# Kernel tuning notes

Hardware: AMD Instinct MI355X
Metric: run time of the kernel (lower is better)

The kernel has to match this reference:

```python
import jax, jax.numpy as jnp
import numpy as np

N_HEADS = 8
N_POINTS = 4
LN_EPS = 1e-5


def _ln(x, g, b):
    m = jnp.mean(x, -1, keepdims=True)
    v = jnp.mean((x - m) ** 2, -1, keepdims=True)
    return (x - m) * jax.lax.rsqrt(v + LN_EPS) * g + b


def _mha(q, k, v, wq, bq, wk, bk, wv, bv, wo, bo):
    B, Lq, C = q.shape
    Dh = C // N_HEADS
    Q = (q @ wq.T + bq).reshape(B, Lq, N_HEADS, Dh)
    K = (k @ wk.T + bk).reshape(B, -1, N_HEADS, Dh)
    V = (v @ wv.T + bv).reshape(B, -1, N_HEADS, Dh)
    s = jnp.einsum('bqhd,bkhd->bhqk', Q, K) * (1.0 / float(np.sqrt(Dh)))
    a = jax.nn.softmax(s, -1)
    o = jnp.einsum('bhqk,bkhd->bqhd', a, V).reshape(B, Lq, C)
    return o @ wo.T + bo


def _ref_points(h, w, L):
    ry = jnp.linspace(0.5, h - 0.5, h) / h
    rx = jnp.linspace(0.5, w - 0.5, w) / w
    gy, gx = jnp.meshgrid(ry, rx, indexing='ij')
    ref = jnp.stack([gx.reshape(-1), gy.reshape(-1)], -1)[None]  # (1, h*w, 2)
    return jnp.broadcast_to(ref[:, :, None, :], (1, h * w, L, 2))


def _deform_core(value, shapes, starts, loc, aw):
    # value: (B, Len_in, H, Dh); loc: (B, Lq, H, L, P, 2); aw: (B, Lq, H, L, P)
    B, _, H, Dh = value.shape
    Lq, P = loc.shape[1], loc.shape[4]
    out = jnp.zeros((B, H, Lq, Dh), value.dtype)
    for l in range(shapes.shape[0]):
        Hl, Wl = int(shapes[l, 0]), int(shapes[l, 1])
        s = int(starts[l])
        v = value[:, s:s + Hl * Wl].transpose(0, 2, 1, 3)  # (B, H, Hl*Wl, Dh)
        # grid_sample(align_corners=False, padding_mode='zeros') pixel coords
        xl = loc[:, :, :, l, :, 0] * Wl - 0.5  # (B, Lq, H, P)
        yl = loc[:, :, :, l, :, 1] * Hl - 0.5
        x0 = jnp.floor(xl); y0 = jnp.floor(yl)
        fx = xl - x0; fy = yl - y0
        x0 = x0.astype(jnp.int32); y0 = y0.astype(jnp.int32)
        acc = jnp.zeros((B, H, Lq, P, Dh), value.dtype)
        for dy, dx in ((0, 0), (0, 1), (1, 0), (1, 1)):
            xi = x0 + dx; yi = y0 + dy
            wgt = (fx if dx else 1.0 - fx) * (fy if dy else 1.0 - fy)
            valid = ((xi >= 0) & (xi < Wl) & (yi >= 0) & (yi < Hl)).astype(value.dtype)
            idx = (jnp.clip(yi, 0, Hl - 1) * Wl + jnp.clip(xi, 0, Wl - 1))
            idx = idx.transpose(0, 2, 1, 3).reshape(B, H, Lq * P)
            g = jnp.take_along_axis(v, idx[..., None], axis=2).reshape(B, H, Lq, P, Dh)
            acc = acc + g * (wgt * valid).transpose(0, 2, 1, 3)[..., None]
        out = out + jnp.einsum('bhqpd,bqhp->bhqd', acc, aw[:, :, :, l])
    return out.transpose(0, 2, 1, 3).reshape(B, Lq, H * Dh)


def reference(tgt, query_pos, src, wq, bq, wk, bk, wv, bv, wo, bo, ln2_g, ln2_b,
              w_off, b_off, w_attn, b_attn, w_val, b_val, w_cout, b_cout,
              ln1_g, ln1_b, w1, b1, w2, b2, ln3_g, ln3_b,
              src_spatial_shapes, level_start_index, h, w):
    shapes = np.asarray(src_spatial_shapes)
    starts = np.asarray(level_start_index)
    h = int(h); w = int(w)
    L = shapes.shape[0]
    B, Lq, C = tgt.shape
    Dh = C // N_HEADS
    # --- self attention (post-LN residual) ---
    q = tgt + query_pos
    t2 = _mha(q, q, tgt, wq, bq, wk, bk, wv, bv, wo, bo)
    t = _ln(tgt + t2, ln2_g, ln2_b)
    # --- MSDeformAttn cross attention ---
    qc = t + query_pos
    value = (src @ w_val.T + b_val).reshape(B, -1, N_HEADS, Dh)
    off = (qc @ w_off.T + b_off).reshape(B, Lq, N_HEADS, L, N_POINTS, 2)
    aw = (qc @ w_attn.T + b_attn).reshape(B, Lq, N_HEADS, L * N_POINTS)
    aw = jax.nn.softmax(aw, -1).reshape(B, Lq, N_HEADS, L, N_POINTS)
    norm = jnp.stack([shapes[:, 1].astype(np.float32), shapes[:, 0].astype(np.float32)], -1)  # (L,2): (W,H)
    rp = _ref_points(h, w, L)  # (1, Lq, L, 2)
    loc = rp[:, :, None, :, None, :] + off / norm[None, None, None, :, None, :]
    samp = _deform_core(value, shapes, starts, loc, aw)
    t2 = samp @ w_cout.T + b_cout
    t = _ln(t + t2, ln1_g, ln1_b)
    # --- FFN ---
    t2 = jax.nn.relu(t @ w1.T + b1) @ w2.T + b2
    t = _ln(t + t2, ln3_g, ln3_b)
    return t


def setup_inputs() -> dict:
    key = jax.random.key(0)
    B, C, L, P, dff = 2, 256, 4, 4, 1024
    h = w = 48
    shapes = np.array([[48, 48], [24, 24], [12, 12], [6, 6]], np.int32)
    starts = np.array([0, 2304, 2880, 3024], np.int32)
    Len_in = 3060
    Lq = h * w
    ks = iter(jax.random.split(key, 40))
    def rn(shape, s=0.02):
        return jax.random.normal(next(ks), shape, jnp.float32) * s
    return dict(
        tgt=rn((B, Lq, C), 1.0), query_pos=rn((B, Lq, C), 1.0), src=rn((B, Len_in, C), 1.0),
        wq=rn((C, C)), bq=rn((C,)), wk=rn((C, C)), bk=rn((C,)), wv=rn((C, C)), bv=rn((C,)),
        wo=rn((C, C)), bo=rn((C,)),
        ln2_g=jnp.ones((C,)), ln2_b=jnp.zeros((C,)),
        w_off=rn((N_HEADS * L * P * 2, C)), b_off=rn((N_HEADS * L * P * 2,)),
        w_attn=rn((N_HEADS * L * P, C)), b_attn=rn((N_HEADS * L * P,)),
        w_val=rn((C, C)), b_val=rn((C,)), w_cout=rn((C, C)), b_cout=rn((C,)),
        ln1_g=jnp.ones((C,)), ln1_b=jnp.zeros((C,)),
        w1=rn((dff, C)), b1=rn((dff,)), w2=rn((C, dff)), b2=rn((C,)),
        ln3_g=jnp.ones((C,)), ln3_b=jnp.zeros((C,)),
        src_spatial_shapes=shapes, level_start_index=starts, h=h, w=w)
```

## Files before the change

### kernel.cpp

```cpp
#include <hip/hip_runtime.h>
#include <hip/hip_bf16.h>
#include <math.h>

typedef __hip_bfloat16 bf16;
typedef __attribute__((ext_vector_type(8))) short short8;
typedef __attribute__((ext_vector_type(4))) short short4v;
typedef __attribute__((ext_vector_type(4))) float f32x4;

static constexpr int B   = 2;
static constexpr int LQ  = 2304;
static constexpr int C   = 256;
static constexpr int NH  = 8;
static constexpr int DH  = 32;
static constexpr int NL  = 4;
static constexpr int NP  = 4;
static constexpr int LEN = 3060;
static constexpr int DFF = 1024;
static constexpr int MQ  = B * LQ;
static constexpr int MV  = B * LEN;
static constexpr int SZ1 = MQ * C;

#define MFMA16(a, b, c) __builtin_amdgcn_mfma_f32_16x16x32_bf16(a, b, c, 0, 0, 0)

__device__ __forceinline__ float ldf(const void* p, size_t i, int bf) {
  return bf ? __bfloat162float(((const bf16*)p)[i]) : ((const float*)p)[i];
}
__device__ __forceinline__ short fl2s(float v) {
  bf16 h = __float2bfloat16(v);
  return *(short*)&h;
}
__device__ __forceinline__ short fl2s_fast(float v) {
  union { float f; unsigned u; } x; x.f = v;
  return (short)((x.u + 0x8000u) >> 16);
}
__device__ __forceinline__ float s2fl(short s) {
  return __bfloat162float(*(bf16*)&s);
}
__device__ __forceinline__ int wire_is_bf16(const unsigned* gprobe) {
  return gprobe[0] == 0x3F803F80u;
}

static constexpr int CVN = 20;
__device__ const int g_cvt_cnt[CVN] = {
  65536, 65536, 256, 256, 65536, 256, 65536, 256,
  65536, 32768, 256, 128, 65536, 256, 65536, 256,
  262144, 1024, 262144, 256};
__device__ const int g_cvt_off[CVN] = {
  0, 65536, 131072, 131328, 131584, 197120, 197376, 262912,
  263168, 328704, 361472, 361728, 361856, 427392, 427648, 493184,
  493440, 755584, 756608, 1018752};
static constexpr int CV_WQ = 0, CV_WK = 65536, CV_BQ = 131072, CV_BK = 131328;
static constexpr int CV_WV = 131584, CV_BV = 197120;
static constexpr int CV_WO = 197376, CV_BO = 262912;
static constexpr int CV_WOFF = 263168, CV_WATTN = 328704;
static constexpr int CV_BOFF = 361472, CV_BATTN = 361728;
static constexpr int CV_WVAL = 361856, CV_BVAL = 427392;
static constexpr int CV_WCOUT = 427648, CV_BCOUT = 493184;
static constexpr int CV_W1 = 493440, CV_B1 = 755584;
static constexpr int CV_W2 = 756608, CV_B2 = 1018752;
static constexpr int CV_TOTAL = 1019008;

struct CvtArgs { const void* p[22]; };

__global__ __launch_bounds__(256) void prep_all(CvtArgs a, const void* __restrict__ qpos,
                                                short* __restrict__ cvt,
                                                short* __restrict__ tgt16,
                                                short* __restrict__ q16,
                                                short* __restrict__ src16,
                                                const unsigned* __restrict__ gprobe) {
  const int fl = wire_is_bf16(gprobe);
  const int seg = blockIdx.y;
  if (fl && seg != 20) return;
  const int cnt = (seg < 20) ? g_cvt_cnt[seg] : (seg == 20 ? SZ1 : MV * C);
  const int stride = gridDim.x * 256;
  for (int i = blockIdx.x * 256 + threadIdx.x; i < cnt; i += stride) {
    if (seg < 20) {
      cvt[g_cvt_off[seg] + i] = fl2s(((const float*)a.p[seg])[i]);
    } else if (seg == 20) {
      float t = ldf(a.p[20], i, fl);
      if (!fl) tgt16[i] = fl2s(t);
      q16[i] = fl2s(t + ldf(qpos, i, fl));
    } else {
      src16[i] = fl2s(((const float*)a.p[21])[i]);
    }
  }
}

struct GemmJob {
  int Xmode;
  const short* Xbf; const void* Xwire;
  const short* Wcvt; const short* bcvt;
  const void* Wwire; const void* bwire;
  void* Y;
  int M, N, K, ldY, col0, relu, out_mode, nblk_x;
  float qscale;
};
struct GemmBatch { GemmJob j[4]; int start[5]; int njobs; };

__global__ __launch_bounds__(256) void gemm_mfma(GemmBatch nb,
                                                 const unsigned* __restrict__ gprobe) {
  const int fl = wire_is_bf16(gprobe);
  int id = blockIdx.x;
  int jj = 0;
  while (jj + 1 < nb.njobs && id >= nb.start[jj + 1]) ++jj;
  const GemmJob jb = nb.j[jj];
  const short* Xsel = (jb.Xmode && fl) ? (const short*)jb.Xwire : jb.Xbf;
  const short* Wsel = fl ? (const short*)jb.Wwire : jb.Wcvt;
  const short* bsel = fl ? (const short*)jb.bwire : jb.bcvt;
  const int local = id - nb.start[jj];
  const int bx = local % jb.nblk_x;
  const int by = local / jb.nblk_x;
  const int M = jb.M, N = jb.N, K = jb.K;

  __shared__ short Xs[128][72];
  __shared__ short Ws[64][72];
  const int tid = threadIdx.x;
  const int wave = tid >> 6, lane = tid & 63;
  const int quad = lane >> 4, l16 = lane & 15;
  const int m0 = bx * 128, n0 = by * 64;
  f32x4 acc[2][4];
#pragma unroll
  for (int mt = 0; mt < 2; ++mt)
#pragma unroll
    for (int nt = 0; nt < 4; ++nt) acc[mt][nt] = f32x4{0.f, 0.f, 0.f, 0.f};

  const int xrow = tid >> 1;
  const int xcol = (tid & 1) * 32;
  const int wrow = tid >> 2;
  const int wcol = (tid & 3) * 16;
  int xr = m0 + xrow; if (xr >= M) xr = M - 1;
  const short* xp = Xsel + (size_t)xr * K;
  const short* wp = Wsel + (size_t)(n0 + wrow) * K;

  for (int k0 = 0; k0 < K; k0 += 64) {
#pragma unroll
    for (int u = 0; u < 4; ++u)
      *(short8*)&Xs[xrow][xcol + u * 8] = *(const short8*)(xp + k0 + xcol + u * 8);
    *(short8*)&Ws[wrow][wcol]     = *(const short8*)(wp + k0 + wcol);
    *(short8*)&Ws[wrow][wcol + 8] = *(const short8*)(wp + k0 + wcol + 8);
    __syncthreads();
#pragma unroll
    for (int kc = 0; kc < 2; ++kc) {
#pragma unroll
      for (int mt = 0; mt < 2; ++mt) {
        short8 a = *(const short8*)&Xs[wave * 32 + mt * 16 + l16][kc * 32 + quad * 8];
#pragma unroll
        for (int nt = 0; nt < 4; ++nt) {
          short8 b = *(const short8*)&Ws[nt * 16 + l16][kc * 32 + quad * 8];
          acc[mt][nt] = MFMA16(a, b, acc[mt][nt]);
        }
      }
    }
    __syncthreads();
  }

  if (jb.out_mode == 2) {
#pragma unroll
    for (int mt = 0; mt < 2; ++mt) {
      const int mbase = m0 + wave * 32 + mt * 16 + quad * 4;
      const int b = mbase / LQ;
      const int qb_ = mbase - b * LQ;
#pragma unroll
      for (int nt = 0; nt < 4; ++nt) {
        const int n = n0 + nt * 16 + l16;
        const float bv = s2fl(bsel[n]);
        short4v v4;
#pragma unroll
        for (int r = 0; r < 4; ++r) v4[r] = fl2s(acc[mt][nt][r] + bv);
        *(short4v*)((short*)jb.Y + (size_t)(b * 256 + n) * LQ + qb_) = v4;
      }
    }
    return;
  }
#pragma unroll
  for (int mt = 0; mt < 2; ++mt)
#pragma unroll
    for (int nt = 0; nt < 4; ++nt) {
      const int n = n0 + nt * 16 + l16;
      const float bv = s2fl(bsel[n]);
#pragma unroll
      for (int r = 0; r < 4; ++r) {
        const int m = m0 + wave * 32 + mt * 16 + quad * 4 + r;
        if (m < M) {
          float v = (acc[mt][nt][r] + bv) * jb.qscale;
          if (jb.relu) v = fmaxf(v, 0.f);
          if (jb.out_mode == 1)
            ((short*)jb.Y)[(size_t)m * jb.ldY + jb.col0 + n] = fl2s(v);
          else
            ((float*)jb.Y)[(size_t)m * jb.ldY + jb.col0 + n] = v;
        }
      }
    }
}

__global__ __launch_bounds__(256) void flash_attn(const short* __restrict__ QK,
                                                  const short* __restrict__ Vt,
                                                  short* __restrict__ Op) {
  constexpr int LDQK = 512;
  constexpr int NC = LQ / 64;
  constexpr int NQT = 3;
  const int qb = blockIdx.x;
  const int bh = blockIdx.y;
  const int b = bh >> 3, h = bh & 7;
  const int tid = threadIdx.x;
  const int wave = tid >> 6, lane = tid & 63;
  const int quad = lane >> 4, l16 = lane & 15;

  __shared__ short Ps[4][16][68];
  __shared__ float lsh[256];

  const int q0 = qb * 48;
  const size_t rowb = (size_t)(b * LQ);
  const short* kcol = QK + 256 + h * DH + quad * 8;
  const short* vt0 = Vt + (size_t)(b * 256 + h * 32 + l16) * LQ + quad * 8;
  const short* vt1 = Vt + (size_t)(b * 256 + h * 32 + 16 + l16) * LQ + quad * 8;

  short8 qfrag[NQT];
#pragma unroll
  for (int qt = 0; qt < NQT; ++qt)
    qfrag[qt] = *(const short8*)(QK + (rowb + q0 + qt * 16 + l16) * LDQK + h * DH + quad * 8);

  f32x4 o0[NQT], o1[NQT];
  float lrow[NQT];
#pragma unroll
  for (int qt = 0; qt < NQT; ++qt) {
    o0[qt] = f32x4{0.f, 0.f, 0.f, 0.f};
    o1[qt] = f32x4{0.f, 0.f, 0.f, 0.f};
    lrow[qt] = 0.f;
  }

  short8 kf[4], vf[4];
  {
    const int k0 = wave * 64;
#pragma unroll
    for (int kt = 0; kt < 4; ++kt)
      kf[kt] = *(const short8*)(kcol + (rowb + k0 + kt * 16 + l16) * LDQK);
    vf[0] = *(const short8*)(vt0 + k0);
    vf[1] = *(const short8*)(vt0 + k0 + 32);
    vf[2] = *(const short8*)(vt1 + k0);
    vf[3] = *(const short8*)(vt1 + k0 + 32);
  }

  for (int c = wave; c < NC; c += 4) {
    short8 kn[4], vn[4];
    if (c + 4 < NC) {
      const int k0n = (c + 4) * 64;
#pragma unroll
      for (int kt = 0; kt < 4; ++kt)
        kn[kt] = *(const short8*)(kcol + (rowb + k0n + kt * 16 + l16) * LDQK);
      vn[0] = *(const short8*)(vt0 + k0n);
      vn[1] = *(const short8*)(vt0 + k0n + 32);
      vn[2] = *(const short8*)(vt1 + k0n);
      vn[3] = *(const short8*)(vt1 + k0n + 32);
    }

#pragma unroll
    for (int qt = 0; qt < NQT; ++qt) {
      f32x4 s[4];
#pragma unroll
      for (int kt = 0; kt < 4; ++kt) {
        f32x4 z = {0.f, 0.f, 0.f, 0.f};
        s[kt] = MFMA16(kf[kt], qfrag[qt], z);
      }

      float ps = 0.f;
#pragma unroll
      for (int kt = 0; kt < 4; ++kt)
#pragma unroll
        for (int r = 0; r < 4; ++r) {
          float p = __expf(s[kt][r]);
          s[kt][r] = p;
          ps += p;
        }
      lrow[qt] += ps;

#pragma unroll
      for (int kt = 0; kt < 4; ++kt) {
        short4v pk;
#pragma unroll
        for (int r = 0; r < 4; ++r) pk[r] = fl2s_fast(s[kt][r]);
        *(short4v*)&Ps[wave][l16][kt * 16 + quad * 4] = pk;
      }

#pragma unroll
      for (int half = 0; half < 2; ++half) {
        short4v a0 = *(const short4v*)&Ps[wave][l16][half * 32 + quad * 8];
        short4v a1 = *(const short4v*)&Ps[wave][l16][half * 32 + quad * 8 + 4];
        short8 afrag;
#pragma unroll
        for (int j = 0; j < 4; ++j) { afrag[j] = a0[j]; afrag[4 + j] = a1[j]; }
        o0[qt] = MFMA16(afrag, vf[half], o0[qt]);
        o1[qt] = MFMA16(afrag, vf[2 + half], o1[qt]);
      }
    }

#pragma unroll
    for (int kt = 0; kt < 4; ++kt) { kf[kt] = kn[kt]; vf[kt] = vn[kt]; }
  }

  float* obuf = (float*)&Ps[0][0][0];
  for (int qt = 0; qt < NQT; ++qt) {
    __syncthreads();
    lsh[(wave * 4 + quad) * 16 + l16] = lrow[qt];
#pragma unroll
    for (int r = 0; r < 4; ++r) {
      const int q = quad * 4 + r;
      obuf[(wave * 16 + q) * 32 + l16] = o0[qt][r];
      obuf[(wave * 16 + q) * 32 + 16 + l16] = o1[qt][r];
    }
    __syncthreads();
#pragma unroll
    for (int e = tid; e < 512; e += 256) {
      const int q = e >> 5, d = e & 31;
      float lg = 0.f;
#pragma unroll
      for (int i = 0; i < 16; ++i) lg += lsh[i * 16 + q];
      float ov = 0.f;
#pragma unroll
      for (int w = 0; w < 4; ++w) ov += obuf[(w * 16 + q) * 32 + d];
      Op[(rowb + q0 + qt * 16 + q) * C + h * DH + d] = fl2s_fast(ov / lg);
    }
  }
}

__global__ __launch_bounds__(256) void ln_kern(const void* __restrict__ A, int a_mode,
                                               const float* __restrict__ R,
                                               const void* __restrict__ g,
                                               const void* __restrict__ be,
                                               float* __restrict__ Yf32,
                                               short* __restrict__ Y16,
                                               void* __restrict__ Yfinal,
                                               const void* __restrict__ pos,
                                               short* __restrict__ Yqc,
                                               int rows, const unsigned* __restrict__ gprobe) {
  const int fl = wire_is_bf16(gprobe);
  const int row = blockIdx.x * 4 + (threadIdx.x >> 6);
  const int lane = threadIdx.x & 63;
  if (row >= rows) return;
  float x[4], s = 0.f, s2 = 0.f;
#pragma unroll
  for (int u = 0; u < 4; ++u) {
    int c = lane + 64 * u;
    size_t idx = (size_t)row * C + c;
    float a = (a_mode == 1) ? ldf(A, idx, fl) : ((const float*)A)[idx];
    x[u] = a + R[idx];
    s += x[u];
    s2 += x[u] * x[u];
  }
#pragma unroll
  for (int off = 32; off > 0; off >>= 1) {
    s += __shfl_xor(s, off);
    s2 += __shfl_xor(s2, off);
  }
  const float mean = s * (1.f / C);
  const float var = fmaxf(s2 * (1.f / C) - mean * mean, 0.f);
  const float inv = rsqrtf(var + 1e-5f);
#pragma unroll
  for (int u = 0; u < 4; ++u) {
    int c = lane + 64 * u;
    size_t idx = (size_t)row * C + c;
    float y = (x[u] - mean) * inv * ldf(g, c, fl) + ldf(be, c, fl);
    if (Yfinal) {
      if (fl) ((short*)Yfinal)[idx] = fl2s(y);
      else ((float*)Yfinal)[idx] = y;
    } else {
      if (Yf32) Yf32[idx] = y;
      if (Y16) Y16[idx] = fl2s(y);
      if (Yqc) Yqc[idx] = fl2s(y + ldf(pos, idx, fl));
    }
  }
}

__global__ __launch_bounds__(256) void deform_kern(const short* __restrict__ value,
                                                   const float* __restrict__ oa,
                                                   const int* __restrict__ shapes,
                                                   const int* __restrict__ starts,
                                                   const int* __restrict__ hp,
                                                   const int* __restrict__ wp,
                                                   short* __restrict__ samp) {
  const int bq = blockIdx.x * 4 + (threadIdx.x >> 6);
  const int b = bq / LQ, q = bq % LQ;
  const int lane = threadIdx.x & 63;
  const int h_ = lane >> 3;
  const int d0 = (lane & 7) * 4;

  const int w0 = *wp, h0 = *hp;
  const int qx = q % w0, qy = q / w0;
  const float refx = (qx + 0.5f) / (float)w0;
  const float refy = (qy + 0.5f) / (float)h0;

  const float* offp = oa + (size_t)bq * 384 + h_ * 32;
  const float* awraw = oa + (size_t)bq * 384 + 256 + h_ * 16;

  float e[16];
  float mm = -1e30f;
#pragma unroll
  for (int j = 0; j < 16; ++j) mm = fmaxf(mm, awraw[j]);
  float ssum = 0.f;
#pragma unroll
  for (int j = 0; j < 16; ++j) {
    e[j] = __expf(awraw[j] - mm);
    ssum += e[j];
  }
  const float sinv = 1.f / ssum;

  float acc0 = 0.f, acc1 = 0.f, acc2 = 0.f, acc3 = 0.f;
  for (int l = 0; l < NL; ++l) {
    const int Hl = shapes[l * 2 + 0];
    const int Wl = shapes[l * 2 + 1];
    const int st = starts[l];
    const short* vbase = value + ((size_t)(b * LEN + st)) * C + h_ * DH + d0;
#pragma unroll
    for (int p = 0; p < NP; ++p) {
      const float ox = offp[l * 8 + p * 2 + 0];
      const float oy = offp[l * 8 + p * 2 + 1];
      const float a = e[l * 4 + p] * sinv;
      const float xl = refx * Wl + ox - 0.5f;
      const float yl = refy * Hl + oy - 0.5f;
      const float x0f = floorf(xl), y0f = floorf(yl);
      const float fx = xl - x0f, fy = yl - y0f;
      const int x0 = (int)x0f, y0 = (int)y0f;
#pragma unroll
      for (int corner = 0; corner < 4; ++corner) {
        const int dx = corner & 1, dy = corner >> 1;
        const int xi = x0 + dx, yi = y0 + dy;
        const float wx = dx ? fx : 1.f - fx;
        const float wy = dy ? fy : 1.f - fy;
        const bool valid = (xi >= 0) & (xi < Wl) & (yi >= 0) & (yi < Hl);
        if (valid) {
          const float w = a * wx * wy;
          short4v v4 = *(const short4v*)(vbase + (size_t)(yi * Wl + xi) * C);
          acc0 += w * s2fl(v4[0]);
          acc1 += w * s2fl(v4[1]);
          acc2 += w * s2fl(v4[2]);
          acc3 += w * s2fl(v4[3]);
        }
      }
    }
  }
  short4v out;
  out[0] = fl2s(acc0); out[1] = fl2s(acc1); out[2] = fl2s(acc2); out[3] = fl2s(acc3);
  *(short4v*)(samp + (size_t)bq * C + h_ * DH + d0) = out;
}

extern "C" void kernel_launch(void* const* d_in, const int* in_sizes, int n_in,
                              void* d_out, int out_size, void* d_ws, size_t ws_size,
                              hipStream_t stream) {
  const void* tgt       = d_in[0];
  const void* query_pos = d_in[1];
  const void* src       = d_in[2];
  const void* wq = d_in[3];  const void* bq = d_in[4];
  const void* wk = d_in[5];  const void* bk = d_in[6];
  const void* wv = d_in[7];  const void* bv = d_in[8];
  const void* wo = d_in[9];  const void* bo = d_in[10];
  const void* ln2_g = d_in[11]; const void* ln2_b = d_in[12];
  const void* w_off = d_in[13]; const void* b_off = d_in[14];
  const void* w_attn = d_in[15]; const void* b_attn = d_in[16];
  const void* w_val = d_in[17]; const void* b_val = d_in[18];
  const void* w_cout = d_in[19]; const void* b_cout = d_in[20];
  const void* ln1_g = d_in[21]; const void* ln1_b = d_in[22];
  const void* w1 = d_in[23]; const void* b1 = d_in[24];
  const void* w2 = d_in[25]; const void* b2 = d_in[26];
  const void* ln3_g = d_in[27]; const void* ln3_b = d_in[28];
  const int* shapes = (const int*)d_in[29];
  const int* starts = (const int*)d_in[30];
  const int* hp = (const int*)d_in[31];
  const int* wp = (const int*)d_in[32];
  const unsigned* gprobe = (const unsigned*)ln2_g;

  short* cvt    = (short*)((char*)d_ws + 256);
  short* tgt16  = cvt + CV_TOTAL;
  short* q16    = tgt16 + SZ1;
  short* src16  = q16 + SZ1;
  short* qk_out = src16 + (size_t)MV * C;
  short* vt16   = qk_out + (size_t)MQ * 512;
  short* ao16   = vt16 + SZ1;
  short* valb   = ao16 + SZ1;
  short* ffn1   = valb + (size_t)MV * C;
  short* t1_16  = ffn1 + (size_t)MQ * DFF;
  float* t2a    = (float*)(t1_16 + SZ1);
  float* t_32   = t2a + SZ1;
  float* t1_32  = t_32 + SZ1;
  float* oa     = t1_32 + SZ1;

  const float scale = 1.f / sqrtf((float)DH);
  const dim3 blk(256);
  const int NXQ = MQ / 128;
  const int NXV = (MV + 127) / 128;

  CvtArgs ca;
  ca.p[0] = wq;  ca.p[1] = wk;  ca.p[2] = bq;  ca.p[3] = bk;
  ca.p[4] = wv;  ca.p[5] = bv;  ca.p[6] = wo;  ca.p[7] = bo;
  ca.p[8] = w_off; ca.p[9] = w_attn; ca.p[10] = b_off; ca.p[11] = b_attn;
  ca.p[12] = w_val; ca.p[13] = b_val; ca.p[14] = w_cout; ca.p[15] = b_cout;
  ca.p[16] = w1; ca.p[17] = b1; ca.p[18] = w2; ca.p[19] = b2;
  ca.p[20] = tgt; ca.p[21] = src;
  prep_all<<<dim3(192, 22), blk, 0, stream>>>(ca, query_pos, cvt, tgt16, q16, src16, gprobe);

  {
    GemmBatch nb;
    nb.njobs = 4;
    nb.j[0] = {0, q16, nullptr, cvt + CV_WQ, cvt + CV_BQ, wq, bq, qk_out,
               MQ, 256, 256, 512, 0, 0, 1, NXQ, scale};
    nb.j[1] = {0, q16, nullptr, cvt + CV_WK, cvt + CV_BK, wk, bk, qk_out,
               MQ, 256, 256, 512, 256, 0, 1, NXQ, 1.f};
    nb.j[2] = {2, tgt16, tgt, cvt + CV_WV, cvt + CV_BV, wv, bv, vt16,
               MQ, 256, 256, 0, 0, 0, 2, NXQ, 1.f};
    nb.j[3] = {3, src16, src, cvt + CV_WVAL, cvt + CV_BVAL, w_val, b_val, valb,
               MV, 256, 256, 256, 0, 0, 1, NXV, 1.f};
    nb.start[0] = 0;
    nb.start[1] = NXQ * 4;
    nb.start[2] = nb.start[1] + NXQ * 4;
    nb.start[3] = nb.start[2] + NXQ * 4;
    nb.start[4] = nb.start[3] + NXV * 4;
    gemm_mfma<<<nb.start[4], blk, 0, stream>>>(nb, gprobe);
  }
  flash_attn<<<dim3(LQ / 48, B * NH), blk, 0, stream>>>(qk_out, vt16, ao16);
  {
    GemmBatch nb;
    nb.njobs = 1;
    nb.j[0] = {0, ao16, nullptr, cvt + CV_WO, cvt + CV_BO, wo, bo, t2a,
               MQ, 256, 256, 256, 0, 0, 0, NXQ, 1.f};
    nb.start[0] = 0; nb.start[1] = NXQ * 4;
    gemm_mfma<<<nb.start[1], blk, 0, stream>>>(nb, gprobe);
  }
  ln_kern<<<MQ / 4, blk, 0, stream>>>(tgt, 1, t2a, ln2_g, ln2_b,
                                      t_32, nullptr, nullptr, query_pos, q16, MQ, gprobe);

  {
    GemmBatch nb;
    nb.njobs = 2;
    nb.j[0] = {0, q16, nullptr, cvt + CV_WOFF, cvt + CV_BOFF, w_off, b_off, oa,
               MQ, 256, 256, 384, 0, 0, 0, NXQ, 1.f};
    nb.j[1] = {0, q16, nullptr, cvt + CV_WATTN, cvt + CV_BATTN, w_attn, b_attn, oa,
               MQ, 128, 256, 384, 256, 0, 0, NXQ, 1.f};
    nb.start[0] = 0;
    nb.start[1] = NXQ * 4;
    nb.start[2] = nb.start[1] + NXQ * 2;
    gemm_mfma<<<nb.start[2], blk, 0, stream>>>(nb, gprobe);
  }
  deform_kern<<<MQ / 4, blk, 0, stream>>>(valb, oa, shapes, starts, hp, wp, ao16);
  {
    GemmBatch nb;
    nb.njobs = 1;
    nb.j[0] = {0, ao16, nullptr, cvt + CV_WCOUT, cvt + CV_BCOUT, w_cout, b_cout, t2a,
               MQ, 256, 256, 256, 0, 0, 0, NXQ, 1.f};
    nb.start[0] = 0; nb.start[1] = NXQ * 4;
    gemm_mfma<<<nb.start[1], blk, 0, stream>>>(nb, gprobe);
  }
  ln_kern<<<MQ / 4, blk, 0, stream>>>(t_32, 2, t2a, ln1_g, ln1_b,
                                      t1_32, t1_16, nullptr, nullptr, nullptr, MQ, gprobe);

  {
    GemmBatch nb;
    nb.njobs = 1;
    nb.j[0] = {0, t1_16, nullptr, cvt + CV_W1, cvt + CV_B1, w1, b1, ffn1,
               MQ, 1024, 256, 1024, 0, 1, 1, NXQ, 1.f};
    nb.start[0] = 0; nb.start[1] = NXQ * 16;
    gemm_mfma<<<nb.start[1], blk, 0, stream>>>(nb, gprobe);
  }
  {
    GemmBatch nb;
    nb.njobs = 1;
    nb.j[0] = {0, ffn1, nullptr, cvt + CV_W2, cvt + CV_B2, w2, b2, t2a,
               MQ, 256, 1024, 256, 0, 0, 0, NXQ, 1.f};
    nb.start[0] = 0; nb.start[1] = NXQ * 4;
    gemm_mfma<<<nb.start[1], blk, 0, stream>>>(nb, gprobe);
  }
  ln_kern<<<MQ / 4, blk, 0, stream>>>(t1_32, 2, t2a, ln3_g, ln3_b,
                                      nullptr, nullptr, d_out, nullptr, nullptr, MQ, gprobe);
}
```

Measured before the change: 284.2 us.

## Fuse tgt+query_pos add into QK GEMM loads and use 64-row tiles for N=256 GEMMs

In bf16-wire mode the prep kernel now exits early. The Q/K projection GEMM reads tgt and query_pos directly and adds them while staging the X tile into shared memory, which removes a separate elementwise pass. The GEMM is templated on its M tile size, and the smaller GEMMs (output projection, offset/attention, cout, FFN2) now use 64-row tiles to launch twice as many blocks for better CU occupancy. The prep grid is also halved. In exchange, each Q/K block redoes the bf16 add per N tile, and smaller tiles reuse each weight tile less.

```diff
diff --git a/kernel.cpp b/kernel.cpp
--- a/kernel.cpp
+++ b/kernel.cpp
@@ -38,6 +38,12 @@
 }
 __device__ __forceinline__ int wire_is_bf16(const unsigned* gprobe) {
   return gprobe[0] == 0x3F803F80u;
+}
+__device__ __forceinline__ short8 add2bf(short8 a, short8 b) {
+  short8 r;
+#pragma unroll
+  for (int j = 0; j < 8; ++j) r[j] = fl2s(s2fl(a[j]) + s2fl(b[j]));
+  return r;
 }
 
 static constexpr int CVN = 20;
@@ -68,18 +74,17 @@
                                                 short* __restrict__ q16,
                                                 short* __restrict__ src16,
                                                 const unsigned* __restrict__ gprobe) {
-  const int fl = wire_is_bf16(gprobe);
+  if (wire_is_bf16(gprobe)) return;
   const int seg = blockIdx.y;
-  if (fl && seg != 20) return;
   const int cnt = (seg < 20) ? g_cvt_cnt[seg] : (seg == 20 ? SZ1 : MV * C);
   const int stride = gridDim.x * 256;
   for (int i = blockIdx.x * 256 + threadIdx.x; i < cnt; i += stride) {
     if (seg < 20) {
       cvt[g_cvt_off[seg] + i] = fl2s(((const float*)a.p[seg])[i]);
     } else if (seg == 20) {
-      float t = ldf(a.p[20], i, fl);
-      if (!fl) tgt16[i] = fl2s(t);
-      q16[i] = fl2s(t + ldf(qpos, i, fl));
+      float t = ((const float*)a.p[20])[i];
+      tgt16[i] = fl2s(t);
+      q16[i] = fl2s(t + ((const float*)qpos)[i]);
     } else {
       src16[i] = fl2s(((const float*)a.p[21])[i]);
     }
@@ -88,7 +93,7 @@
 
 struct GemmJob {
   int Xmode;
-  const short* Xbf; const void* Xwire;
+  const short* Xbf; const void* Xwire; const void* Xwire2;
   const short* Wcvt; const short* bcvt;
   const void* Wwire; const void* bwire;
   void* Y;
@@ -97,14 +102,18 @@
 };
 struct GemmBatch { GemmJob j[4]; int start[5]; int njobs; };
 
+template <int MR>
 __global__ __launch_bounds__(256) void gemm_mfma(GemmBatch nb,
                                                  const unsigned* __restrict__ gprobe) {
+  constexpr int MT = MR / 64;
   const int fl = wire_is_bf16(gprobe);
   int id = blockIdx.x;
   int jj = 0;
   while (jj + 1 < nb.njobs && id >= nb.start[jj + 1]) ++jj;
   const GemmJob jb = nb.j[jj];
-  const short* Xsel = (jb.Xmode && fl) ? (const short*)jb.Xwire : jb.Xbf;
+  const bool qcf = (jb.Xmode == 4) && fl;
+  const short* Xsel = jb.Xbf;
+  if ((jb.Xmode == 2 || jb.Xmode == 3) && fl) Xsel = (const short*)jb.Xwire;
   const short* Wsel = fl ? (const short*)jb.Wwire : jb.Wcvt;
   const short* bsel = fl ? (const short*)jb.bwire : jb.bcvt;
   const int local = id - nb.start[jj];
@@ -112,38 +121,50 @@
   const int by = local / jb.nblk_x;
   const int M = jb.M, N = jb.N, K = jb.K;
 
-  __shared__ short Xs[128][72];
+  __shared__ short Xs[MR][72];
   __shared__ short Ws[64][72];
   const int tid = threadIdx.x;
   const int wave = tid >> 6, lane = tid & 63;
   const int quad = lane >> 4, l16 = lane & 15;
-  const int m0 = bx * 128, n0 = by * 64;
-  f32x4 acc[2][4];
-#pragma unroll
-  for (int mt = 0; mt < 2; ++mt)
+  const int m0 = bx * MR, n0 = by * 64;
+  f32x4 acc[MT][4];
+#pragma unroll
+  for (int mt = 0; mt < MT; ++mt)
 #pragma unroll
     for (int nt = 0; nt < 4; ++nt) acc[mt][nt] = f32x4{0.f, 0.f, 0.f, 0.f};
 
-  const int xrow = tid >> 1;
-  const int xcol = (tid & 1) * 32;
+  const int xrow = (MR == 128) ? (tid >> 1) : (tid >> 2);
+  const int xcol = (MR == 128) ? ((tid & 1) * 32) : ((tid & 3) * 16);
+  constexpr int XU = (MR == 128) ? 4 : 2;
   const int wrow = tid >> 2;
   const int wcol = (tid & 3) * 16;
   int xr = m0 + xrow; if (xr >= M) xr = M - 1;
-  const short* xp = Xsel + (size_t)xr * K;
+  const short* xp = qcf ? nullptr : (Xsel + (size_t)xr * K);
+  const short* tp = qcf ? ((const short*)jb.Xwire + (size_t)xr * K) : nullptr;
+  const short* pp = qcf ? ((const short*)jb.Xwire2 + (size_t)xr * K) : nullptr;
   const short* wp = Wsel + (size_t)(n0 + wrow) * K;
 
   for (int k0 = 0; k0 < K; k0 += 64) {
-#pragma unroll
-    for (int u = 0; u < 4; ++u)
-      *(short8*)&Xs[xrow][xcol + u * 8] = *(const short8*)(xp + k0 + xcol + u * 8);
+    if (qcf) {
+#pragma unroll
+      for (int u = 0; u < XU; ++u) {
+        short8 t8 = *(const short8*)(tp + k0 + xcol + u * 8);
+        short8 p8 = *(const short8*)(pp + k0 + xcol + u * 8);
+        *(short8*)&Xs[xrow][xcol + u * 8] = add2bf(t8, p8);
+      }
+    } else {
+#pragma unroll
+      for (int u = 0; u < XU; ++u)
+        *(short8*)&Xs[xrow][xcol + u * 8] = *(const short8*)(xp + k0 + xcol + u * 8);
+    }
     *(short8*)&Ws[wrow][wcol]     = *(const short8*)(wp + k0 + wcol);
     *(short8*)&Ws[wrow][wcol + 8] = *(const short8*)(wp + k0 + wcol + 8);
     __syncthreads();
 #pragma unroll
     for (int kc = 0; kc < 2; ++kc) {
 #pragma unroll
-      for (int mt = 0; mt < 2; ++mt) {
-        short8 a = *(const short8*)&Xs[wave * 32 + mt * 16 + l16][kc * 32 + quad * 8];
+      for (int mt = 0; mt < MT; ++mt) {
+        short8 a = *(const short8*)&Xs[wave * (16 * MT) + mt * 16 + l16][kc * 32 + quad * 8];
 #pragma unroll
         for (int nt = 0; nt < 4; ++nt) {
           short8 b = *(const short8*)&Ws[nt * 16 + l16][kc * 32 + quad * 8];
@@ -156,8 +177,8 @@
 
   if (jb.out_mode == 2) {
 #pragma unroll
-    for (int mt = 0; mt < 2; ++mt) {
-      const int mbase = m0 + wave * 32 + mt * 16 + quad * 4;
+    for (int mt = 0; mt < MT; ++mt) {
+      const int mbase = m0 + wave * (16 * MT) + mt * 16 + quad * 4;
       const int b = mbase / LQ;
       const int qb_ = mbase - b * LQ;
 #pragma unroll
@@ -173,14 +194,14 @@
     return;
   }
 #pragma unroll
-  for (int mt = 0; mt < 2; ++mt)
+  for (int mt = 0; mt < MT; ++mt)
 #pragma unroll
     for (int nt = 0; nt < 4; ++nt) {
       const int n = n0 + nt * 16 + l16;
       const float bv = s2fl(bsel[n]);
 #pragma unroll
       for (int r = 0; r < 4; ++r) {
-        const int m = m0 + wave * 32 + mt * 16 + quad * 4 + r;
+        const int m = m0 + wave * (16 * MT) + mt * 16 + quad * 4 + r;
         if (m < M) {
           float v = (acc[mt][nt][r] + bv) * jb.qscale;
           if (jb.relu) v = fmaxf(v, 0.f);
@@ -485,8 +506,9 @@
 
   const float scale = 1.f / sqrtf((float)DH);
   const dim3 blk(256);
-  const int NXQ = MQ / 128;
-  const int NXV = (MV + 127) / 128;
+  const int NX128 = MQ / 128;
+  const int NX64  = MQ / 64;
+  const int NXV   = (MV + 127) / 128;
 
   CvtArgs ca;
   ca.p[0] = wq;  ca.p[1] = wk;  ca.p[2] = bq;  ca.p[3] = bk;
@@ -495,34 +517,34 @@
   ca.p[12] = w_val; ca.p[13] = b_val; ca.p[14] = w_cout; ca.p[15] = b_cout;
   ca.p[16] = w1; ca.p[17] = b1; ca.p[18] = w2; ca.p[19] = b2;
   ca.p[20] = tgt; ca.p[21] = src;
-  prep_all<<<dim3(192, 22), blk, 0, stream>>>(ca, query_pos, cvt, tgt16, q16, src16, gprobe);
+  prep_all<<<dim3(96, 22), blk, 0, stream>>>(ca, query_pos, cvt, tgt16, q16, src16, gprobe);
 
   {
     GemmBatch nb;
     nb.njobs = 4;
-    nb.j[0] = {0, q16, nullptr, cvt + CV_WQ, cvt + CV_BQ, wq, bq, qk_out,
-               MQ, 256, 256, 512, 0, 0, 1, NXQ, scale};
-    nb.j[1] = {0, q16, nullptr, cvt + CV_WK, cvt + CV_BK, wk, bk, qk_out,
-               MQ, 256, 256, 512, 256, 0, 1, NXQ, 1.f};
-    nb.j[2] = {2, tgt16, tgt, cvt + CV_WV, cvt + CV_BV, wv, bv, vt16,
-               MQ, 256, 256, 0, 0, 0, 2, NXQ, 1.f};
-    nb.j[3] = {3, src16, src, cvt + CV_WVAL, cvt + CV_BVAL, w_val, b_val, valb,
+    nb.j[0] = {4, q16, tgt, query_pos, cvt + CV_WQ, cvt + CV_BQ, wq, bq, qk_out,
+               MQ, 256, 256, 512, 0, 0, 1, NX128, scale};
+    nb.j[1] = {4, q16, tgt, query_pos, cvt + CV_WK, cvt + CV_BK, wk, bk, qk_out,
+               MQ, 256, 256, 512, 256, 0, 1, NX128, 1.f};
+    nb.j[2] = {2, tgt16, tgt, nullptr, cvt + CV_WV, cvt + CV_BV, wv, bv, vt16,
+               MQ, 256, 256, 0, 0, 0, 2, NX128, 1.f};
+    nb.j[3] = {3, src16, src, nullptr, cvt + CV_WVAL, cvt + CV_BVAL, w_val, b_val, valb,
                MV, 256, 256, 256, 0, 0, 1, NXV, 1.f};
     nb.start[0] = 0;
-    nb.start[1] = NXQ * 4;
-    nb.start[2] = nb.start[1] + NXQ * 4;
-    nb.start[3] = nb.start[2] + NXQ * 4;
+    nb.start[1] = NX128 * 4;
+    nb.start[2] = nb.start[1] + NX128 * 4;
+    nb.start[3] = nb.start[2] + NX128 * 4;
     nb.start[4] = nb.start[3] + NXV * 4;
-    gemm_mfma<<<nb.start[4], blk, 0, stream>>>(nb, gprobe);
+    gemm_mfma<128><<<nb.start[4], blk, 0, stream>>>(nb, gprobe);
   }
   flash_attn<<<dim3(LQ / 48, B * NH), blk, 0, stream>>>(qk_out, vt16, ao16);
   {
     GemmBatch nb;
     nb.njobs = 1;
-    nb.j[0] = {0, ao16, nullptr, cvt + CV_WO, cvt + CV_BO, wo, bo, t2a,
-               MQ, 256, 256, 256, 0, 0, 0, NXQ, 1.f};
-    nb.start[0] = 0; nb.start[1] = NXQ * 4;
-    gemm_mfma<<<nb.start[1], blk, 0, stream>>>(nb, gprobe);
+    nb.j[0] = {0, ao16, nullptr, nullptr, cvt + CV_WO, cvt + CV_BO, wo, bo, t2a,
+               MQ, 256, 256, 256, 0, 0, 0, NX64, 1.f};
+    nb.start[0] = 0; nb.start[1] = NX64 * 4;
+    gemm_mfma<64><<<nb.start[1], blk, 0, stream>>>(nb, gprobe);
   }
   ln_kern<<<MQ / 4, blk, 0, stream>>>(tgt, 1, t2a, ln2_g, ln2_b,
                                       t_32, nullptr, nullptr, query_pos, q16, MQ, gprobe);
@@ -530,23 +552,23 @@
   {
     GemmBatch nb;
     nb.njobs = 2;
-    nb.j[0] = {0, q16, nullptr, cvt + CV_WOFF, cvt + CV_BOFF, w_off, b_off, oa,
-               MQ, 256, 256, 384, 0, 0, 0, NXQ, 1.f};
-    nb.j[1] = {0, q16, nullptr, cvt + CV_WATTN, cvt + CV_BATTN, w_attn, b_attn, oa,
-               MQ, 128, 256, 384, 256, 0, 0, NXQ, 1.f};
+    nb.j[0] = {0, q16, nullptr, nullptr, cvt + CV_WOFF, cvt + CV_BOFF, w_off, b_off, oa,
+               MQ, 256, 256, 384, 0, 0, 0, NX64, 1.f};
+    nb.j[1] = {0, q16, nullptr, nullptr, cvt + CV_WATTN, cvt + CV_BATTN, w_attn, b_attn, oa,
+               MQ, 128, 256, 384, 256, 0, 0, NX64, 1.f};
     nb.start[0] = 0;
-    nb.start[1] = NXQ * 4;
-    nb.start[2] = nb.start[1] + NXQ * 2;
-    gemm_mfma<<<nb.start[2], blk, 0, stream>>>(nb, gprobe);
+    nb.start[1] = NX64 * 4;
+    nb.start[2] = nb.start[1] + NX64 * 2;
+    gemm_mfma<64><<<nb.start[2], blk, 0, stream>>>(nb, gprobe);
   }
   deform_kern<<<MQ / 4, blk, 0, stream>>>(valb, oa, shapes, starts, hp, wp, ao16);
   {
     GemmBatch nb;
     nb.njobs = 1;
-    nb.j[0] = {0, ao16, nullptr, cvt + CV_WCOUT, cvt + CV_BCOUT, w_cout, b_cout, t2a,
-               MQ, 256, 256, 256, 0, 0, 0, NXQ, 1.f};
-    nb.start[0] = 0; nb.start[1] = NXQ * 4;
-    gemm_mfma<<<nb.start[1], blk, 0, stream>>>(nb, gprobe);
+    nb.j[0] = {0, ao16, nullptr, nullptr, cvt + CV_WCOUT, cvt + CV_BCOUT, w_cout, b_cout, t2a,
+               MQ, 256, 256, 256, 0, 0, 0, NX64, 1.f};
+    nb.start[0] = 0; nb.start[1] = NX64 * 4;
+    gemm_mfma<64><<<nb.start[1], blk, 0, stream>>>(nb, gprobe);
   }
   ln_kern<<<MQ / 4, blk, 0, stream>>>(t_32, 2, t2a, ln1_g, ln1_b,
                                       t1_32, t1_16, nullptr, nullptr, nullptr, MQ, gprobe);
@@ -554,18 +576,18 @@
   {
     GemmBatch nb;
     nb.njobs = 1;
-    nb.j[0] = {0, t1_16, nullptr, cvt + CV_W1, cvt + CV_B1, w1, b1, ffn1,
-               MQ, 1024, 256, 1024, 0, 1, 1, NXQ, 1.f};
-    nb.start[0] = 0; nb.start[1] = NXQ * 16;
-    gemm_mfma<<<nb.start[1], blk, 0, stream>>>(nb, gprobe);
+    nb.j[0] = {0, t1_16, nullptr, nullptr, cvt + CV_W1, cvt + CV_B1, w1, b1, ffn1,
+               MQ, 1024, 256, 1024, 0, 1, 1, NX128, 1.f};
+    nb.start[0] = 0; nb.start[1] = NX128 * 16;
+    gemm_mfma<128><<<nb.start[1], blk, 0, stream>>>(nb, gprobe);
   }
   {
     GemmBatch nb;
     nb.njobs = 1;
-    nb.j[0] = {0, ffn1, nullptr, cvt + CV_W2, cvt + CV_B2, w2, b2, t2a,
-               MQ, 256, 1024, 256, 0, 0, 0, NXQ, 1.f};
-    nb.start[0] = 0; nb.start[1] = NXQ * 4;
-    gemm_mfma<<<nb.start[1], blk, 0, stream>>>(nb, gprobe);
+    nb.j[0] = {0, ffn1, nullptr, nullptr, cvt + CV_W2, cvt + CV_B2, w2, b2, t2a,
+               MQ, 256, 1024, 256, 0, 0, 0, NX64, 1.f};
+    nb.start[0] = 0; nb.start[1] = NX64 * 4;
+    gemm_mfma<64><<<nb.start[1], blk, 0, stream>>>(nb, gprobe);
   }
   ln_kern<<<MQ / 4, blk, 0, stream>>>(t1_32, 2, t2a, ln3_g, ln3_b,
                                       nullptr, nullptr, d_out, nullptr, nullptr, MQ, gprobe);
```

After: 284.2 us (median of 2 runs). Within noise of the previous version (-0.0%).
